# Kernel tuning notes

Hardware: AMD Instinct MI355X
Metric: run time of the kernel (lower is better)

## Reference

```python
import jax, jax.numpy as jnp
import numpy as np

B, C, H, W = 32, 256, 64, 64
N_HEAD, LDIM = 4, 64
HW = H * W
SCALE = float(np.sqrt(LDIM))
EPS = 1e-5


def setup_inputs() -> dict:
    key = jax.random.key(0)
    ks = jax.random.split(key, 8)
    inp = {
        "x": jax.random.normal(ks[0], (B, C, H, W), dtype=jnp.float32),
        "x1": jax.random.normal(ks[1], (B, C, H, W), dtype=jnp.float32),
        # linear weights stored as [in, out] (transposed torch layout)
        "Wq": jax.random.normal(ks[2], (HW, N_HEAD * LDIM), dtype=jnp.float32) * 0.02,
        "Wk": jax.random.normal(ks[3], (HW, N_HEAD * LDIM), dtype=jnp.float32) * 0.02,
        "Wv": jax.random.normal(ks[4], (HW, N_HEAD * LDIM), dtype=jnp.float32) * 0.02,
        "Wfc": jax.random.normal(ks[5], (N_HEAD * LDIM, HW), dtype=jnp.float32) * 0.02,
        "gamma": jnp.ones((C,), dtype=jnp.float32),
        "beta": jnp.zeros((C,), dtype=jnp.float32),
    }
    return inp


def reference(x, x1, Wq, Wk, Wv, Wfc, gamma, beta):
    b, c, h, w = x.shape
    xf = x.reshape(b, c, h * w)    # [b, c, hw]
    x1f = x1.reshape(b, c, h * w)
    # projections: [b, c, hw] @ [hw, n*d] -> [b, c, n*d]
    q = (xf @ Wq).reshape(b, c, N_HEAD, LDIM).transpose(0, 2, 1, 3)   # [b, n, c, d]
    k = (x1f @ Wk).reshape(b, c, N_HEAD, LDIM).transpose(0, 2, 1, 3)
    v = (x1f @ Wv).reshape(b, c, N_HEAD, LDIM).transpose(0, 2, 1, 3)
    # scaled dot-product attention over the c 'channel-token' axis
    attn = jnp.einsum('bncd,bnmd->bncm', q / SCALE, k)  # [b, n, c, c]
    attn = jax.nn.softmax(attn, axis=-1)
    out = jnp.einsum('bncm,bnmd->bncd', attn, v)        # [b, n, c, d]
    out = out.transpose(0, 2, 1, 3).reshape(b, c, N_HEAD * LDIM)
    out = (out @ Wfc).reshape(b, c, h, w)
    # BatchNorm2d (training-mode batch statistics, biased variance)
    mean = out.mean(axis=(0, 2, 3), keepdims=True)
    var = out.var(axis=(0, 2, 3), keepdims=True)
    out = (out - mean) * jax.lax.rsqrt(var + EPS)
    out = out * gamma[None, :, None, None] + beta[None, :, None, None]
    return out
```

## Files before the change

kernel.cpp:

```cpp
#include <hip/hip_runtime.h>
#include <hip/hip_bf16.h>

#define Bsz 32
#define Csz 256
#define HWsz 4096
#define NDsz 256
#define Msz 8192

typedef __bf16 bf16x8 __attribute__((ext_vector_type(8)));
typedef float  f32x4  __attribute__((ext_vector_type(4)));
typedef short  s16x4  __attribute__((ext_vector_type(4)));
typedef short  s16x8  __attribute__((ext_vector_type(8)));

__device__ __forceinline__ unsigned short f2bf(float f){
  unsigned u = __float_as_uint(f);
  u += 0x7FFFu + ((u >> 16) & 1u);
  return (unsigned short)(u >> 16);
}

__device__ __forceinline__ f32x4 mfma16(bf16x8 a, bf16x8 b, f32x4 c){
  return __builtin_amdgcn_mfma_f32_16x16x32_bf16(a, b, c, 0, 0, 0);
}

__global__ void k_prep(const float* __restrict__ Wq, const float* __restrict__ Wk,
                       const float* __restrict__ Wv, const float* __restrict__ Wfc,
                       unsigned short* __restrict__ Wt, unsigned short* __restrict__ Wfct){
  __shared__ float t[32][33];
  int z = blockIdx.z;
  int bx = blockIdx.x, by = blockIdx.y;
  const float* src; unsigned short* dst; int R, Ct;
  if (z < 3) {
    src = (z == 0) ? Wq : (z == 1 ? Wk : Wv);
    dst = Wt + (size_t)z * Csz * HWsz;  R = HWsz; Ct = NDsz;
  } else {
    int tidx = bx * 8 + by; bx = tidx & 7; by = tidx >> 3;
    src = Wfc; dst = Wfct; R = NDsz; Ct = HWsz;
  }
  int tx = threadIdx.x, ty = threadIdx.y;
  int i0 = bx * 32, j0 = by * 32;
  #pragma unroll
  for (int r = 0; r < 4; r++)
    t[ty + 8*r][tx] = src[(size_t)(i0 + ty + 8*r) * Ct + j0 + tx];
  __syncthreads();
  #pragma unroll
  for (int r = 0; r < 4; r++)
    dst[(size_t)(j0 + ty + 8*r) * R + i0 + tx] = f2bf(t[tx][ty + 8*r]);
}

__global__ __launch_bounds__(256) void k_proj(const float* __restrict__ X,
    const float* __restrict__ X1, const unsigned short* __restrict__ Wt,
    unsigned short* __restrict__ QKV){
  const int which = blockIdx.x;
  const int rt = blockIdx.y;
  const float* A = (which == 0) ? X : X1;
  const unsigned short* Bt = Wt + (size_t)which * NDsz * HWsz;
  unsigned short* Cp = QKV + (size_t)which * Msz * NDsz;

  __shared__ unsigned short As[64][72];
  __shared__ unsigned short Bs[256][72];

  const int tid = threadIdx.x;
  const int lane = tid & 63, w = tid >> 6;
  const int l15 = lane & 15, l4 = lane >> 4;

  const int arow = tid >> 2, acol = (tid & 3) * 16;
  const float* agp = A + (size_t)(rt*64 + arow) * HWsz + acol;
  const int brow = tid >> 3, bcol = (tid & 7) * 8;
  const unsigned short* bgp = Bt + (size_t)brow * HWsz + bcol;

  f32x4 acc[4][4] = {};
  float4 ar[4];
  s16x8 br[8];

#define LOADA(kt) { _Pragma("unroll") for (int i = 0; i < 4; i++) \
    ar[i] = *(const float4*)(agp + (size_t)(kt)*64 + i*4); }
#define LOADB(kt) { _Pragma("unroll") for (int p = 0; p < 8; p++) \
    br[p] = *(const s16x8*)(bgp + (size_t)p*32*HWsz + (size_t)(kt)*64); }
#define WRITEAB { _Pragma("unroll") for (int i = 0; i < 4; i++){ s16x4 cv; \
      cv[0]=(short)f2bf(ar[i].x); cv[1]=(short)f2bf(ar[i].y); \
      cv[2]=(short)f2bf(ar[i].z); cv[3]=(short)f2bf(ar[i].w); \
      *(s16x4*)&As[arow][acol + i*4] = cv; } \
    _Pragma("unroll") for (int p = 0; p < 8; p++) *(s16x8*)&Bs[p*32 + brow][bcol] = br[p]; }

  LOADA(0); LOADB(0);
  WRITEAB;
  __syncthreads();

  const int NK = HWsz / 64;
  for (int kt = 1; kt <= NK; kt++){
    const bool more = (kt < NK);
    if (more){ LOADA(kt); LOADB(kt); }
    #pragma unroll
    for (int kk = 0; kk < 2; kk++){
      bf16x8 a[4], b[4];
      #pragma unroll
      for (int fm = 0; fm < 4; fm++) a[fm] = *(const bf16x8*)&As[fm*16 + l15][kk*32 + l4*8];
      #pragma unroll
      for (int fn = 0; fn < 4; fn++) b[fn] = *(const bf16x8*)&Bs[w*64 + fn*16 + l15][kk*32 + l4*8];
      #pragma unroll
      for (int fm = 0; fm < 4; fm++)
        #pragma unroll
        for (int fn = 0; fn < 4; fn++)
          acc[fm][fn] = mfma16(a[fm], b[fn], acc[fm][fn]);
    }
    if (more){
      __syncthreads();
      WRITEAB;
      __syncthreads();
    }
  }
#undef LOADA
#undef LOADB
#undef WRITEAB
  #pragma unroll
  for (int fm = 0; fm < 4; fm++)
    #pragma unroll
    for (int fn = 0; fn < 4; fn++)
      #pragma unroll
      for (int r = 0; r < 4; r++)
        Cp[(size_t)(rt*64 + fm*16 + l4*4 + r) * NDsz + w*64 + fn*16 + l15] =
            f2bf(acc[fm][fn][r]);
}

__global__ __launch_bounds__(256) void k_attn(const unsigned short* __restrict__ Q,
    const unsigned short* __restrict__ K, const unsigned short* __restrict__ V,
    unsigned short* __restrict__ O){
  const int b = blockIdx.x >> 2, n = blockIdx.x & 3;
  __shared__ unsigned short VT[64][264];
  __shared__ unsigned short PL[4][64][72];

  const int tid = threadIdx.x;
  const int lane = tid & 63, w = tid >> 6;
  const int l15 = lane & 15, l4 = lane >> 4;

  {
    const unsigned short* vp = V + (size_t)(b*256 + tid) * NDsz + n*64;
    #pragma unroll
    for (int j = 0; j < 8; j++){
      s16x8 vv = *(const s16x8*)(vp + j*8);
      #pragma unroll
      for (int e = 0; e < 8; e++) VT[j*8 + e][tid] = (unsigned short)vv[e];
    }
  }

  bf16x8 qf[4][2];
  #pragma unroll
  for (int fm = 0; fm < 4; fm++)
    #pragma unroll
    for (int ks = 0; ks < 2; ks++)
      qf[fm][ks] = *(const bf16x8*)(Q + (size_t)(b*256 + w*64 + fm*16 + l15) * NDsz
                                      + n*64 + ks*32 + l4*8);

  f32x4 oacc[4][4] = {};
  float rs[4][4] = {};
  __syncthreads();

  for (int ch = 0; ch < 4; ch++){
    f32x4 sacc[4][4] = {};
    #pragma unroll
    for (int ks = 0; ks < 2; ks++){
      bf16x8 kf[4];
      #pragma unroll
      for (int fn = 0; fn < 4; fn++)
        kf[fn] = *(const bf16x8*)(K + (size_t)(b*256 + ch*64 + fn*16 + l15) * NDsz
                                    + n*64 + ks*32 + l4*8);
      #pragma unroll
      for (int fm = 0; fm < 4; fm++)
        #pragma unroll
        for (int fn = 0; fn < 4; fn++)
          sacc[fm][fn] = mfma16(qf[fm][ks], kf[fn], sacc[fm][fn]);
    }
    #pragma unroll
    for (int fm = 0; fm < 4; fm++)
      #pragma unroll
      for (int fn = 0; fn < 4; fn++)
        #pragma unroll
        for (int r = 0; r < 4; r++){
          float e = __expf(sacc[fm][fn][r] * 0.125f);
          rs[fm][r] += e;
          PL[w][fm*16 + l4*4 + r][fn*16 + l15] = f2bf(e);
        }
    #pragma unroll
    for (int ks = 0; ks < 2; ks++){
      bf16x8 pa[4], vb[4];
      #pragma unroll
      for (int fm = 0; fm < 4; fm++)
        pa[fm] = *(const bf16x8*)&PL[w][fm*16 + l15][ks*32 + l4*8];
      #pragma unroll
      for (int fn = 0; fn < 4; fn++)
        vb[fn] = *(const bf16x8*)&VT[fn*16 + l15][ch*64 + ks*32 + l4*8];
      #pragma unroll
      for (int fm = 0; fm < 4; fm++)
        #pragma unroll
        for (int fn = 0; fn < 4; fn++)
          oacc[fm][fn] = mfma16(pa[fm], vb[fn], oacc[fm][fn]);
    }
  }
  #pragma unroll
  for (int fm = 0; fm < 4; fm++)
    #pragma unroll
    for (int r = 0; r < 4; r++){
      float s = rs[fm][r];
      s += __shfl_xor(s, 1, 16); s += __shfl_xor(s, 2, 16);
      s += __shfl_xor(s, 4, 16); s += __shfl_xor(s, 8, 16);
      rs[fm][r] = 1.0f / s;
    }
  #pragma unroll
  for (int fm = 0; fm < 4; fm++)
    #pragma unroll
    for (int fn = 0; fn < 4; fn++)
      #pragma unroll
      for (int r = 0; r < 4; r++)
        O[(size_t)(b*256 + w*64 + fm*16 + l4*4 + r) * NDsz + n*64 + fn*16 + l15] =
            f2bf(oacc[fm][fn][r] * rs[fm][r]);
}

__global__ __launch_bounds__(256) void k_fc(const unsigned short* __restrict__ AO,
    const unsigned short* __restrict__ Wfct, float* __restrict__ Y){
  const int ct = blockIdx.x, rt = blockIdx.y;
  __shared__ union UU {
    struct { unsigned short As[64][72]; unsigned short Bs[256][72]; } st;
    float Cs[4][64][68];
  } u;
  const int tid = threadIdx.x;
  const int lane = tid & 63, w = tid >> 6;
  const int l15 = lane & 15, l4 = lane >> 4;

  const int arow = tid >> 2, acol = (tid & 3) * 16;
  const unsigned short* agp = AO + (size_t)(rt*64 + arow) * NDsz + acol;
  const int brow = tid >> 3, bcol = (tid & 7) * 8;
  const unsigned short* bgp = Wfct + (size_t)(ct*256 + brow) * NDsz + bcol;

  f32x4 acc[4][4] = {};
  s16x8 ar2[2];
  s16x8 br[8];

#define LOADA(kt) { _Pragma("unroll") for (int i = 0; i < 2; i++) \
    ar2[i] = *(const s16x8*)(agp + (kt)*64 + i*8); }
#define LOADB(kt) { _Pragma("unroll") for (int p = 0; p < 8; p++) \
    br[p] = *(const s16x8*)(bgp + (size_t)p*32*NDsz + (kt)*64); }
#define WRITEAB { _Pragma("unroll") for (int i = 0; i < 2; i++) \
    *(s16x8*)&u.st.As[arow][acol + i*8] = ar2[i]; \
    _Pragma("unroll") for (int p = 0; p < 8; p++) *(s16x8*)&u.st.Bs[p*32 + brow][bcol] = br[p]; }

  LOADA(0); LOADB(0);
  WRITEAB;
  __syncthreads();

  const int NK = NDsz / 64;
  for (int kt = 1; kt <= NK; kt++){
    const bool more = (kt < NK);
    if (more){ LOADA(kt); LOADB(kt); }
    #pragma unroll
    for (int kk = 0; kk < 2; kk++){
      bf16x8 a[4], b[4];
      #pragma unroll
      for (int fm = 0; fm < 4; fm++) a[fm] = *(const bf16x8*)&u.st.As[fm*16 + l15][kk*32 + l4*8];
      #pragma unroll
      for (int fn = 0; fn < 4; fn++) b[fn] = *(const bf16x8*)&u.st.Bs[w*64 + fn*16 + l15][kk*32 + l4*8];
      #pragma unroll
      for (int fm = 0; fm < 4; fm++)
        #pragma unroll
        for (int fn = 0; fn < 4; fn++)
          acc[fm][fn] = mfma16(a[fm], b[fn], acc[fm][fn]);
    }
    if (more){
      __syncthreads();
      WRITEAB;
      __syncthreads();
    }
  }
#undef LOADA
#undef LOADB
#undef WRITEAB
  __syncthreads();
  #pragma unroll
  for (int fm = 0; fm < 4; fm++)
    #pragma unroll
    for (int fn = 0; fn < 4; fn++)
      #pragma unroll
      for (int r = 0; r < 4; r++)
        u.Cs[w][fm*16 + l4*4 + r][fn*16 + l15] = acc[fm][fn][r];
  #pragma unroll
  for (int i = 0; i < 16; i++){
    int linear = i*64 + lane;
    int row = linear >> 4, f4 = linear & 15;
    float4 v = *(const float4*)&u.Cs[w][row][f4*4];
    *(float4*)(Y + (size_t)(rt*64 + row) * HWsz + ct*256 + w*64 + f4*4) = v;
  }
}

__global__ __launch_bounds__(256) void k_stats(const float* __restrict__ Y,
    const float* __restrict__ gamma, const float* __restrict__ beta,
    float* __restrict__ scale, float* __restrict__ shift){
  const int c = blockIdx.x, t = threadIdx.x;
  float s = 0.f, sq = 0.f;
  for (int b = 0; b < Bsz; b++){
    const float4* p = (const float4*)(Y + (size_t)(b*Csz + c) * HWsz);
    #pragma unroll
    for (int i = 0; i < 4; i++){
      float4 v = p[t + i*256];
      s  += v.x + v.y + v.z + v.w;
      sq += v.x*v.x + v.y*v.y + v.z*v.z + v.w*v.w;
    }
  }
  __shared__ float ls[256], lq[256];
  ls[t] = s; lq[t] = sq;
  __syncthreads();
  for (int o = 128; o > 0; o >>= 1){
    if (t < o){ ls[t] += ls[t+o]; lq[t] += lq[t+o]; }
    __syncthreads();
  }
  if (t == 0){
    const float inv = 1.0f / (float)(Bsz * HWsz);
    float mean = ls[0] * inv;
    float var  = lq[0] * inv - mean*mean;
    float istd = rsqrtf(var + 1e-5f);
    float g = gamma[c] * istd;
    scale[c] = g;
    shift[c] = beta[c] - mean * g;
  }
}

__global__ __launch_bounds__(256) void k_apply(float* __restrict__ Y,
    const float* __restrict__ scale, const float* __restrict__ shift){
  const int NF4 = Msz * HWsz / 4;
  int gstride = gridDim.x * blockDim.x;
  for (int F = blockIdx.x * blockDim.x + threadIdx.x; F < NF4; F += gstride){
    int c = (F >> 10) & 255;
    float4 v = ((const float4*)Y)[F];
    float sc = scale[c], sh = shift[c];
    v.x = v.x*sc + sh; v.y = v.y*sc + sh; v.z = v.z*sc + sh; v.w = v.w*sc + sh;
    ((float4*)Y)[F] = v;
  }
}

extern "C" void kernel_launch(void* const* d_in, const int* in_sizes, int n_in,
                              void* d_out, int out_size, void* d_ws, size_t ws_size,
                              hipStream_t stream){
  const float* x     = (const float*)d_in[0];
  const float* x1    = (const float*)d_in[1];
  const float* Wq    = (const float*)d_in[2];
  const float* Wk    = (const float*)d_in[3];
  const float* Wv    = (const float*)d_in[4];
  const float* Wfc   = (const float*)d_in[5];
  const float* gamma = (const float*)d_in[6];
  const float* beta  = (const float*)d_in[7];
  float* Y = (float*)d_out;

  unsigned short* Wt   = (unsigned short*)d_ws;
  unsigned short* Wfct = Wt + (size_t)3*Csz*HWsz;
  unsigned short* QKV  = Wfct + (size_t)HWsz*NDsz;
  unsigned short* AO   = QKV + (size_t)3*Msz*NDsz;
  float* scale = (float*)(AO + (size_t)Msz*NDsz);
  float* shift = scale + 256;

  k_prep <<<dim3(128, 8, 4), dim3(32, 8), 0, stream>>>(Wq, Wk, Wv, Wfc, Wt, Wfct);
  k_proj <<<dim3(3, 128),    dim3(256),   0, stream>>>(x, x1, Wt, QKV);
  k_attn <<<dim3(128),       dim3(256),   0, stream>>>(QKV, QKV + (size_t)Msz*NDsz,
                                                       QKV + (size_t)2*Msz*NDsz, AO);
  k_fc   <<<dim3(16, 128),   dim3(256),   0, stream>>>(AO, Wfct, Y);
  k_stats<<<dim3(256),       dim3(256),   0, stream>>>(Y, gamma, beta, scale, shift);
  k_apply<<<dim3(2048),      dim3(256),   0, stream>>>(Y, scale, shift);
}
```

Before: 525.2 us.

## Fuse BatchNorm statistics into FC epilogue and retile projection and attention grids

BatchNorm per-row sum and sum-of-squares are now reduced in the FC GEMM epilogue through wave shuffles, shared memory and atomics. A tiny reduction kernel then produces scale and shift, so the separate full read of Y for statistics is gone. The projection GEMM is split into 128-column tiles with an XCD-aware block mapping, launching 768 blocks instead of 384. Attention is split into two halves over query rows, launching 256 blocks instead of 128. This raises parallelism at the cost of more redundant A and K/V reads, atomic contention, and a memset.

```diff
diff --git a/kernel.cpp b/kernel.cpp
--- a/kernel.cpp
+++ b/kernel.cpp
@@ -47,40 +47,45 @@
     dst[(size_t)(j0 + ty + 8*r) * R + i0 + tx] = f2bf(t[tx][ty + 8*r]);
 }
 
-__global__ __launch_bounds__(256) void k_proj(const float* __restrict__ X,
+__global__ __launch_bounds__(256, 3) void k_proj(const float* __restrict__ X,
     const float* __restrict__ X1, const unsigned short* __restrict__ Wt,
     unsigned short* __restrict__ QKV){
-  const int which = blockIdx.x;
-  const int rt = blockIdx.y;
+  const int wgid = blockIdx.x;
+  const int xcd = wgid & 7, q = wgid >> 3;
+  const int rtHi = q / 6, m = q - rtHi * 6;
+  const int rt = rtHi * 8 + xcd;
+  const int which = m >> 1, ct = m & 1;
+
   const float* A = (which == 0) ? X : X1;
   const unsigned short* Bt = Wt + (size_t)which * NDsz * HWsz;
   unsigned short* Cp = QKV + (size_t)which * Msz * NDsz;
 
   __shared__ unsigned short As[64][72];
-  __shared__ unsigned short Bs[256][72];
+  __shared__ unsigned short Bs[128][72];
 
   const int tid = threadIdx.x;
   const int lane = tid & 63, w = tid >> 6;
   const int l15 = lane & 15, l4 = lane >> 4;
+  const int wm = w >> 1, wn = w & 1;
 
   const int arow = tid >> 2, acol = (tid & 3) * 16;
   const float* agp = A + (size_t)(rt*64 + arow) * HWsz + acol;
-  const int brow = tid >> 3, bcol = (tid & 7) * 8;
-  const unsigned short* bgp = Bt + (size_t)brow * HWsz + bcol;
-
-  f32x4 acc[4][4] = {};
+  const int brow = tid >> 1, bcol = (tid & 1) * 32;
+  const unsigned short* bgp = Bt + (size_t)(ct*128 + brow) * HWsz + bcol;
+
+  f32x4 acc[2][4] = {};
   float4 ar[4];
-  s16x8 br[8];
+  s16x8 br[4];
 
 #define LOADA(kt) { _Pragma("unroll") for (int i = 0; i < 4; i++) \
     ar[i] = *(const float4*)(agp + (size_t)(kt)*64 + i*4); }
-#define LOADB(kt) { _Pragma("unroll") for (int p = 0; p < 8; p++) \
-    br[p] = *(const s16x8*)(bgp + (size_t)p*32*HWsz + (size_t)(kt)*64); }
+#define LOADB(kt) { _Pragma("unroll") for (int p = 0; p < 4; p++) \
+    br[p] = *(const s16x8*)(bgp + (size_t)(kt)*64 + p*8); }
 #define WRITEAB { _Pragma("unroll") for (int i = 0; i < 4; i++){ s16x4 cv; \
       cv[0]=(short)f2bf(ar[i].x); cv[1]=(short)f2bf(ar[i].y); \
       cv[2]=(short)f2bf(ar[i].z); cv[3]=(short)f2bf(ar[i].w); \
       *(s16x4*)&As[arow][acol + i*4] = cv; } \
-    _Pragma("unroll") for (int p = 0; p < 8; p++) *(s16x8*)&Bs[p*32 + brow][bcol] = br[p]; }
+    _Pragma("unroll") for (int p = 0; p < 4; p++) *(s16x8*)&Bs[brow][bcol + p*8] = br[p]; }
 
   LOADA(0); LOADB(0);
   WRITEAB;
@@ -92,13 +97,13 @@
     if (more){ LOADA(kt); LOADB(kt); }
     #pragma unroll
     for (int kk = 0; kk < 2; kk++){
-      bf16x8 a[4], b[4];
-      #pragma unroll
-      for (int fm = 0; fm < 4; fm++) a[fm] = *(const bf16x8*)&As[fm*16 + l15][kk*32 + l4*8];
-      #pragma unroll
-      for (int fn = 0; fn < 4; fn++) b[fn] = *(const bf16x8*)&Bs[w*64 + fn*16 + l15][kk*32 + l4*8];
-      #pragma unroll
-      for (int fm = 0; fm < 4; fm++)
+      bf16x8 a[2], b[4];
+      #pragma unroll
+      for (int fm = 0; fm < 2; fm++) a[fm] = *(const bf16x8*)&As[wm*32 + fm*16 + l15][kk*32 + l4*8];
+      #pragma unroll
+      for (int fn = 0; fn < 4; fn++) b[fn] = *(const bf16x8*)&Bs[wn*64 + fn*16 + l15][kk*32 + l4*8];
+      #pragma unroll
+      for (int fm = 0; fm < 2; fm++)
         #pragma unroll
         for (int fn = 0; fn < 4; fn++)
           acc[fm][fn] = mfma16(a[fm], b[fn], acc[fm][fn]);
@@ -113,21 +118,21 @@
 #undef LOADB
 #undef WRITEAB
   #pragma unroll
-  for (int fm = 0; fm < 4; fm++)
+  for (int fm = 0; fm < 2; fm++)
     #pragma unroll
     for (int fn = 0; fn < 4; fn++)
       #pragma unroll
       for (int r = 0; r < 4; r++)
-        Cp[(size_t)(rt*64 + fm*16 + l4*4 + r) * NDsz + w*64 + fn*16 + l15] =
-            f2bf(acc[fm][fn][r]);
+        Cp[(size_t)(rt*64 + wm*32 + fm*16 + l4*4 + r) * NDsz
+           + ct*128 + wn*64 + fn*16 + l15] = f2bf(acc[fm][fn][r]);
 }
 
 __global__ __launch_bounds__(256) void k_attn(const unsigned short* __restrict__ Q,
     const unsigned short* __restrict__ K, const unsigned short* __restrict__ V,
     unsigned short* __restrict__ O){
-  const int b = blockIdx.x >> 2, n = blockIdx.x & 3;
+  const int b = blockIdx.x >> 3, n = (blockIdx.x >> 1) & 3, half = blockIdx.x & 1;
   __shared__ unsigned short VT[64][264];
-  __shared__ unsigned short PL[4][64][72];
+  __shared__ unsigned short PL[4][32][72];
 
   const int tid = threadIdx.x;
   const int lane = tid & 63, w = tid >> 6;
@@ -143,20 +148,21 @@
     }
   }
 
-  bf16x8 qf[4][2];
-  #pragma unroll
-  for (int fm = 0; fm < 4; fm++)
+  const int qbase = b*256 + half*128 + w*32;
+  bf16x8 qf[2][2];
+  #pragma unroll
+  for (int fm = 0; fm < 2; fm++)
     #pragma unroll
     for (int ks = 0; ks < 2; ks++)
-      qf[fm][ks] = *(const bf16x8*)(Q + (size_t)(b*256 + w*64 + fm*16 + l15) * NDsz
+      qf[fm][ks] = *(const bf16x8*)(Q + (size_t)(qbase + fm*16 + l15) * NDsz
                                       + n*64 + ks*32 + l4*8);
 
-  f32x4 oacc[4][4] = {};
-  float rs[4][4] = {};
+  f32x4 oacc[2][4] = {};
+  float rs[2][4] = {};
   __syncthreads();
 
   for (int ch = 0; ch < 4; ch++){
-    f32x4 sacc[4][4] = {};
+    f32x4 sacc[2][4] = {};
     #pragma unroll
     for (int ks = 0; ks < 2; ks++){
       bf16x8 kf[4];
@@ -165,13 +171,13 @@
         kf[fn] = *(const bf16x8*)(K + (size_t)(b*256 + ch*64 + fn*16 + l15) * NDsz
                                     + n*64 + ks*32 + l4*8);
       #pragma unroll
-      for (int fm = 0; fm < 4; fm++)
+      for (int fm = 0; fm < 2; fm++)
         #pragma unroll
         for (int fn = 0; fn < 4; fn++)
           sacc[fm][fn] = mfma16(qf[fm][ks], kf[fn], sacc[fm][fn]);
     }
     #pragma unroll
-    for (int fm = 0; fm < 4; fm++)
+    for (int fm = 0; fm < 2; fm++)
       #pragma unroll
       for (int fn = 0; fn < 4; fn++)
         #pragma unroll
@@ -182,22 +188,22 @@
         }
     #pragma unroll
     for (int ks = 0; ks < 2; ks++){
-      bf16x8 pa[4], vb[4];
-      #pragma unroll
-      for (int fm = 0; fm < 4; fm++)
+      bf16x8 pa[2], vb[4];
+      #pragma unroll
+      for (int fm = 0; fm < 2; fm++)
         pa[fm] = *(const bf16x8*)&PL[w][fm*16 + l15][ks*32 + l4*8];
       #pragma unroll
       for (int fn = 0; fn < 4; fn++)
         vb[fn] = *(const bf16x8*)&VT[fn*16 + l15][ch*64 + ks*32 + l4*8];
       #pragma unroll
-      for (int fm = 0; fm < 4; fm++)
+      for (int fm = 0; fm < 2; fm++)
         #pragma unroll
         for (int fn = 0; fn < 4; fn++)
           oacc[fm][fn] = mfma16(pa[fm], vb[fn], oacc[fm][fn]);
     }
   }
   #pragma unroll
-  for (int fm = 0; fm < 4; fm++)
+  for (int fm = 0; fm < 2; fm++)
     #pragma unroll
     for (int r = 0; r < 4; r++){
       float s = rs[fm][r];
@@ -206,22 +212,24 @@
       rs[fm][r] = 1.0f / s;
     }
   #pragma unroll
-  for (int fm = 0; fm < 4; fm++)
+  for (int fm = 0; fm < 2; fm++)
     #pragma unroll
     for (int fn = 0; fn < 4; fn++)
       #pragma unroll
       for (int r = 0; r < 4; r++)
-        O[(size_t)(b*256 + w*64 + fm*16 + l4*4 + r) * NDsz + n*64 + fn*16 + l15] =
+        O[(size_t)(qbase + fm*16 + l4*4 + r) * NDsz + n*64 + fn*16 + l15] =
             f2bf(oacc[fm][fn][r] * rs[fm][r]);
 }
 
 __global__ __launch_bounds__(256) void k_fc(const unsigned short* __restrict__ AO,
-    const unsigned short* __restrict__ Wfct, float* __restrict__ Y){
+    const unsigned short* __restrict__ Wfct, float* __restrict__ Y,
+    float* __restrict__ rowsum, float* __restrict__ rowsq){
   const int ct = blockIdx.x, rt = blockIdx.y;
   __shared__ union UU {
     struct { unsigned short As[64][72]; unsigned short Bs[256][72]; } st;
     float Cs[4][64][68];
   } u;
+  __shared__ float sRow[4][64], sRowQ[4][64];
   const int tid = threadIdx.x;
   const int lane = tid & 63, w = tid >> 6;
   const int l15 = lane & 15, l4 = lane >> 4;
@@ -273,7 +281,31 @@
 #undef LOADA
 #undef LOADB
 #undef WRITEAB
-  __syncthreads();
+  float prs[4][4], prq[4][4];
+  #pragma unroll
+  for (int fm = 0; fm < 4; fm++)
+    #pragma unroll
+    for (int r = 0; r < 4; r++){
+      float s = 0.f, qq = 0.f;
+      #pragma unroll
+      for (int fn = 0; fn < 4; fn++){ float v = acc[fm][fn][r]; s += v; qq += v*v; }
+      s  += __shfl_xor(s, 1, 16);  s += __shfl_xor(s, 2, 16);
+      s  += __shfl_xor(s, 4, 16);  s += __shfl_xor(s, 8, 16);
+      qq += __shfl_xor(qq, 1, 16); qq += __shfl_xor(qq, 2, 16);
+      qq += __shfl_xor(qq, 4, 16); qq += __shfl_xor(qq, 8, 16);
+      prs[fm][r] = s; prq[fm][r] = qq;
+    }
+  __syncthreads();
+  if (l15 == 0){
+    #pragma unroll
+    for (int fm = 0; fm < 4; fm++)
+      #pragma unroll
+      for (int r = 0; r < 4; r++){
+        int row = fm*16 + l4*4 + r;
+        sRow[w][row]  = prs[fm][r];
+        sRowQ[w][row] = prq[fm][r];
+      }
+  }
   #pragma unroll
   for (int fm = 0; fm < 4; fm++)
     #pragma unroll
@@ -281,6 +313,13 @@
       #pragma unroll
       for (int r = 0; r < 4; r++)
         u.Cs[w][fm*16 + l4*4 + r][fn*16 + l15] = acc[fm][fn][r];
+  __syncthreads();
+  if (tid < 64){
+    float s = sRow[0][tid] + sRow[1][tid] + sRow[2][tid] + sRow[3][tid];
+    float qq = sRowQ[0][tid] + sRowQ[1][tid] + sRowQ[2][tid] + sRowQ[3][tid];
+    atomicAdd(&rowsum[rt*64 + tid], s);
+    atomicAdd(&rowsq[rt*64 + tid], qq);
+  }
   #pragma unroll
   for (int i = 0; i < 16; i++){
     int linear = i*64 + lane;
@@ -290,31 +329,29 @@
   }
 }
 
-__global__ __launch_bounds__(256) void k_stats(const float* __restrict__ Y,
-    const float* __restrict__ gamma, const float* __restrict__ beta,
-    float* __restrict__ scale, float* __restrict__ shift){
-  const int c = blockIdx.x, t = threadIdx.x;
-  float s = 0.f, sq = 0.f;
-  for (int b = 0; b < Bsz; b++){
-    const float4* p = (const float4*)(Y + (size_t)(b*Csz + c) * HWsz);
-    #pragma unroll
-    for (int i = 0; i < 4; i++){
-      float4 v = p[t + i*256];
-      s  += v.x + v.y + v.z + v.w;
-      sq += v.x*v.x + v.y*v.y + v.z*v.z + v.w*v.w;
-    }
-  }
-  __shared__ float ls[256], lq[256];
-  ls[t] = s; lq[t] = sq;
-  __syncthreads();
-  for (int o = 128; o > 0; o >>= 1){
-    if (t < o){ ls[t] += ls[t+o]; lq[t] += lq[t+o]; }
-    __syncthreads();
-  }
-  if (t == 0){
+__global__ __launch_bounds__(256) void k_bnred(const float* __restrict__ rowsum,
+    const float* __restrict__ rowsq, const float* __restrict__ gamma,
+    const float* __restrict__ beta, float* __restrict__ scale,
+    float* __restrict__ shift){
+  const int t = threadIdx.x;
+  const int c = blockIdx.x * 32 + (t & 31);
+  const int part = t >> 5;
+  float s = 0.f, qq = 0.f;
+  #pragma unroll
+  for (int j = 0; j < 4; j++){
+    int row = (part*4 + j) * 256 + c;
+    s += rowsum[row]; qq += rowsq[row];
+  }
+  __shared__ float ls[8][32], lq[8][32];
+  ls[part][t & 31] = s; lq[part][t & 31] = qq;
+  __syncthreads();
+  if (t < 32){
+    float S = 0.f, Q = 0.f;
+    #pragma unroll
+    for (int p = 0; p < 8; p++){ S += ls[p][t]; Q += lq[p][t]; }
     const float inv = 1.0f / (float)(Bsz * HWsz);
-    float mean = ls[0] * inv;
-    float var  = lq[0] * inv - mean*mean;
+    float mean = S * inv;
+    float var  = Q * inv - mean*mean;
     float istd = rsqrtf(var + 1e-5f);
     float g = gamma[c] * istd;
     scale[c] = g;
@@ -352,14 +389,18 @@
   unsigned short* Wfct = Wt + (size_t)3*Csz*HWsz;
   unsigned short* QKV  = Wfct + (size_t)HWsz*NDsz;
   unsigned short* AO   = QKV + (size_t)3*Msz*NDsz;
-  float* scale = (float*)(AO + (size_t)Msz*NDsz);
-  float* shift = scale + 256;
+  float* rowsum = (float*)(AO + (size_t)Msz*NDsz);
+  float* rowsq  = rowsum + Msz;
+  float* scale  = rowsq + Msz;
+  float* shift  = scale + 256;
+
+  hipMemsetAsync(rowsum, 0, 2 * Msz * sizeof(float), stream);
 
   k_prep <<<dim3(128, 8, 4), dim3(32, 8), 0, stream>>>(Wq, Wk, Wv, Wfc, Wt, Wfct);
-  k_proj <<<dim3(3, 128),    dim3(256),   0, stream>>>(x, x1, Wt, QKV);
-  k_attn <<<dim3(128),       dim3(256),   0, stream>>>(QKV, QKV + (size_t)Msz*NDsz,
+  k_proj <<<dim3(768),       dim3(256),   0, stream>>>(x, x1, Wt, QKV);
+  k_attn <<<dim3(256),       dim3(256),   0, stream>>>(QKV, QKV + (size_t)Msz*NDsz,
                                                        QKV + (size_t)2*Msz*NDsz, AO);
-  k_fc   <<<dim3(16, 128),   dim3(256),   0, stream>>>(AO, Wfct, Y);
-  k_stats<<<dim3(256),       dim3(256),   0, stream>>>(Y, gamma, beta, scale, shift);
+  k_fc   <<<dim3(16, 128),   dim3(256),   0, stream>>>(AO, Wfct, Y, rowsum, rowsq);
+  k_bnred<<<dim3(8),         dim3(256),   0, stream>>>(rowsum, rowsq, gamma, beta, scale, shift);
   k_apply<<<dim3(2048),      dim3(256),   0, stream>>>(Y, scale, shift);
 }
```

Measured after the change: 549.3 us. 4.6% more time.
